# Performance work log

Measured on AMD Instinct MI355X. Metric: run time of the kernel, lower is better.

## Reference

```python
import jax, jax.numpy as jnp
import numpy as np
import math

ROPE_THETA = 10000.0

def apply_rope(t, pos, theta):
    # t: [b, h, s, d_k] with d_k even; pos: [b, s] int
    d_k = t.shape[-1]
    inv_freq = theta ** (-jnp.arange(0, d_k, 2, dtype=jnp.float32) / d_k)  # [d_k/2]
    angles = pos.astype(jnp.float32)[..., None] * inv_freq  # [b, s, d_k/2]
    cos = jnp.cos(angles)[:, None, :, :]  # [b, 1, s, d_k/2]
    sin = jnp.sin(angles)[:, None, :, :]
    t_even = t[..., 0::2]
    t_odd = t[..., 1::2]
    out_even = cos * t_even - sin * t_odd
    out_odd = sin * t_even + cos * t_odd
    # interleave back: [..., d_k/2, 2] -> [..., d_k]
    return jnp.stack([out_even, out_odd], axis=-1).reshape(t.shape)

def setup_inputs() -> dict:
    key = jax.random.key(0)
    k1, k2, k3, k4, k5 = jax.random.split(key, 5)
    b, s, d_model = 2, 2048, 1024
    std = math.sqrt(2.0 / (2 * d_model))
    return {
        "x": jax.random.normal(k1, (b, s, d_model), dtype=jnp.float32),
        "token_positions": jnp.broadcast_to(jnp.arange(s, dtype=jnp.int32), (b, s)),
        "W_Q": jax.random.normal(k2, (d_model, d_model), dtype=jnp.float32) * std,
        "W_K": jax.random.normal(k3, (d_model, d_model), dtype=jnp.float32) * std,
        "W_V": jax.random.normal(k4, (d_model, d_model), dtype=jnp.float32) * std,
        "W_O": jax.random.normal(k5, (d_model, d_model), dtype=jnp.float32) * std,
    }

def reference(x, token_positions, W_Q, W_K, W_V, W_O):
    b, s, d_model = x.shape
    n_heads = 16
    d_k = d_model // n_heads

    def proj(W):
        # x @ W^T then split heads: [b, s, d_model] -> [b, h, s, d_k]
        y = jnp.einsum('bsd,ed->bse', x, W)
        return y.reshape(b, s, n_heads, d_k).transpose(0, 2, 1, 3)

    Q = apply_rope(proj(W_Q), token_positions, ROPE_THETA)
    K = apply_rope(proj(W_K), token_positions, ROPE_THETA)
    V = proj(W_V)

    scores = jnp.einsum('bhqd,bhkd->bhqk', Q, K) / math.sqrt(d_k)
    causal = jnp.tril(jnp.ones((s, s), dtype=bool))  # True = keep
    scores = jnp.where(causal, scores, -jnp.inf)
    attn = jax.nn.softmax(scores, axis=-1)
    out = jnp.einsum('bhqk,bhkd->bhqd', attn, V)
    out = out.transpose(0, 2, 1, 3).reshape(b, s, d_model)  # merge heads
    return jnp.einsum('bse,de->bsd', out, W_O)
```

## Files before the change

### kernel.cpp

```cpp
#include <hip/hip_runtime.h>
#include <hip/hip_bf16.h>

typedef __attribute__((ext_vector_type(8))) short short8;
typedef __attribute__((ext_vector_type(4))) short short4v;
typedef __attribute__((ext_vector_type(4))) float f32x4;

#define LN10000_DIV32 0.2878231366242558f
#define SCALE_Q_LOG2E 0.18033688011112042f
#define EXP_BIAS 12.0f

__device__ __forceinline__ unsigned short f2bf(float f){
  union { float fv; unsigned u; } a; a.fv = f;
  return (unsigned short)((a.u + 0x7fffu + ((a.u >> 16) & 1u)) >> 16);
}

__global__ __launch_bounds__(256) void convert_all(
    const float* __restrict__ x, const float* __restrict__ wq,
    const float* __restrict__ wk, const float* __restrict__ wv,
    const float* __restrict__ wo, unsigned short* __restrict__ dst,
    float2* __restrict__ tab)
{
  size_t t = (size_t)blockIdx.x * 256 + threadIdx.x;
  if (t < 65536UL){
    const int s = (int)(t >> 5), ip = (int)(t & 31);
    float invf = __expf(-(float)ip * LN10000_DIV32);
    float ang = (float)s * invf;
    tab[t] = make_float2(__cosf(ang), __sinf(ang));
  }
  size_t e = t * 8;
  const float* src; size_t off;
  if (e < 4194304UL)      { src = x;  off = e; }
  else if (e < 5242880UL) { src = wq; off = e - 4194304UL; }
  else if (e < 6291456UL) { src = wk; off = e - 5242880UL; }
  else if (e < 7340032UL) { src = wv; off = e - 6291456UL; }
  else                    { src = wo; off = e - 7340032UL; }
  float4 f0 = *(const float4*)(src + off);
  float4 f1 = *(const float4*)(src + off + 4);
  short8 o;
  o[0] = (short)f2bf(f0.x); o[1] = (short)f2bf(f0.y);
  o[2] = (short)f2bf(f0.z); o[3] = (short)f2bf(f0.w);
  o[4] = (short)f2bf(f1.x); o[5] = (short)f2bf(f1.y);
  o[6] = (short)f2bf(f1.z); o[7] = (short)f2bf(f1.w);
  *(short8*)(dst + e) = o;
}

__global__ __launch_bounds__(512, 2) void gemm_qkv(
    const unsigned short* __restrict__ Xb, const unsigned short* __restrict__ Wb,
    const int* __restrict__ positions, const float2* __restrict__ tab,
    unsigned short* __restrict__ Qb, unsigned short* __restrict__ Kb,
    unsigned short* __restrict__ Vtb)
{
  __shared__ __align__(16) unsigned short As[2*8192];
  __shared__ __align__(16) unsigned short Bs[2*12288];
  f32x4 acc[4][3] = {};
  const int tid = threadIdx.x, lane = tid & 63, w = tid >> 6;
  const int wm = w >> 2, wn = w & 3;
  const int fr = lane & 15, fq = lane >> 4;
  const int id  = blockIdx.x;
  const int xcd = id & 7;
  const int lid = id >> 3;
  const int m0 = (lid & 31) * 128;
  const int n0 = (xcd*2 + (lid >> 5)) * 192;

#define STAGE_ALL(kt, buf) do {                                                     \
    _Pragma("unroll")                                                               \
    for (int i_ = 0; i_ < 2; ++i_){                             \
      const int c_ = i_*512 + tid;                                                  \
      const int row_ = c_ >> 3, cd_ = c_ & 7;                                       \
      const int sc_ = (cd_ ^ (row_ & 7)) << 3;                                      \
      const unsigned short* ga_ = Xb + (size_t)(m0 + row_) * 1024 + (kt)*64 + sc_;  \
      __builtin_amdgcn_global_load_lds((const __attribute__((address_space(1))) void*)ga_, \
          (__attribute__((address_space(3))) void*)(As + (buf)*8192 + c_*8), 16, 0, 0);    \
    }                                                                               \
    _Pragma("unroll")                                                               \
    for (int i_ = 0; i_ < 3; ++i_){                             \
      const int c_ = i_*512 + tid;                                                  \
      const int row_ = c_ >> 3, cd_ = c_ & 7;                                       \
      const int sc_ = (cd_ ^ (row_ & 7)) << 3;                                      \
      const unsigned short* gb_ = Wb + (size_t)(n0 + row_) * 1024 + (kt)*64 + sc_;  \
      __builtin_amdgcn_global_load_lds((const __attribute__((address_space(1))) void*)gb_, \
          (__attribute__((address_space(3))) void*)(Bs + (buf)*12288 + c_*8), 16, 0, 0);   \
    }                                                                               \
  } while(0)

  STAGE_ALL(0, 0);

  const int row_a0 = wm*64 + fr;
  const int row_b0 = wn*48 + fr;

  for (int t = 0; t < 16; ++t){
    const int cur = t & 1;
    if (t + 1 < 16){
      STAGE_ALL(t + 1, cur ^ 1);
      asm volatile("s_waitcnt vmcnt(5)" ::: "memory");
    } else {
      asm volatile("s_waitcnt vmcnt(0)" ::: "memory");
    }
    __builtin_amdgcn_s_barrier();
    asm volatile("" ::: "memory");
    const unsigned short* as = As + cur*8192;
    const unsigned short* bs = Bs + cur*12288;
    short8 af[4], bfv[3];

#define LDA(mf_, kh_) do { \
      const int row_ = row_a0 + (mf_)*16; \
      const int c_ = ((kh_)*4 + fq) ^ (row_ & 7); \
      af[mf_] = *(const short8*)(as + row_*64 + c_*8); } while(0)
#define LDB(nf_, kh_) do { \
      const int row_ = row_b0 + (nf_)*16; \
      const int c_ = ((kh_)*4 + fq) ^ (row_ & 7); \
      bfv[nf_] = *(const short8*)(bs + row_*64 + c_*8); } while(0)

    LDA(0,0); LDA(1,0); LDA(2,0); LDA(3,0);
    LDB(0,0); LDB(1,0); LDB(2,0);
    __builtin_amdgcn_s_setprio(1);
    #pragma unroll
    for (int mf = 0; mf < 4; ++mf)
      #pragma unroll
      for (int nf = 0; nf < 3; ++nf)
        acc[mf][nf] = __builtin_amdgcn_mfma_f32_16x16x32_bf16(af[mf], bfv[nf], acc[mf][nf], 0, 0, 0);
    __builtin_amdgcn_s_setprio(0);

    LDA(0,1); LDA(1,1); LDA(2,1); LDA(3,1);
    LDB(0,1); LDB(1,1); LDB(2,1);
    __builtin_amdgcn_s_setprio(1);
    #pragma unroll
    for (int mf = 0; mf < 4; ++mf)
      #pragma unroll
      for (int nf = 0; nf < 3; ++nf)
        acc[mf][nf] = __builtin_amdgcn_mfma_f32_16x16x32_bf16(af[mf], bfv[nf], acc[mf][nf], 0, 0, 0);
    __builtin_amdgcn_s_setprio(0);
    asm volatile("" ::: "memory");
    __builtin_amdgcn_s_barrier();
#undef LDA
#undef LDB
  }
#undef STAGE_ALL

  #pragma unroll
  for (int mf = 0; mf < 4; ++mf){
    int pm[4];
    #pragma unroll
    for (int r = 0; r < 4; ++r){
      const int m = m0 + wm*64 + mf*16 + fq*4 + r;
      pm[r] = positions[m] & 2047;
    }
    const int mbase = m0 + wm*64 + mf*16 + fq*4;
    const int b = mbase >> 11;
    const int s0 = mbase & 2047;
    #pragma unroll
    for (int nf = 0; nf < 3; ++nf){
      const int n = n0 + wn*48 + nf*16 + fr;
      const int seg = n >> 10;
      const int h = (n & 1023) >> 6, d = n & 63;
      const size_t bh = (size_t)b * 16 + h;
      if (seg == 2){
        short4v pack;
        #pragma unroll
        for (int r = 0; r < 4; ++r)
          pack[r] = (short)f2bf(acc[mf][nf][r]);
        *(short4v*)&Vtb[(bh*64 + d)*2048 + s0] = pack;
      } else {
        const int ip = d >> 1;
        #pragma unroll
        for (int r = 0; r < 4; ++r){
          float v = acc[mf][nf][r];
          float pv = __shfl_xor(v, 1);
          const float2 cs = tab[(pm[r] << 5) + ip];
          float outv = (d & 1) ? (cs.x * v + cs.y * pv)
                               : (cs.x * v - cs.y * pv);
          if (seg == 0) outv *= SCALE_Q_LOG2E;
          const unsigned short ob = f2bf(outv);
          const int s = s0 + r;
          if (seg == 0) Qb[(bh*2048 + s)*64 + d] = ob;
          else          Kb[(bh*2048 + s)*64 + d] = ob;
        }
      }
    }
  }
}

__global__ __launch_bounds__(256) void attn_kernel(
    const unsigned short* __restrict__ Qb, const unsigned short* __restrict__ Kb,
    const unsigned short* __restrict__ Vtb, unsigned short* __restrict__ Ob)
{
  __shared__ __align__(16) unsigned short Ks[2][4096];
  __shared__ __align__(16) unsigned short Vs[2][4096];
  __shared__ __align__(16) unsigned short Plds[4][16][64];

  const int tid = threadIdx.x, lane = tid & 63, w = tid >> 6;
  const int fr = lane & 15, fq = lane >> 4;

  const int i = blockIdx.x;
  const int bh = (i & 7) | (((i >> 3) & 3) << 3);
  const int tile = 31 - (i >> 5);
  const int b = bh >> 4, h = bh & 15;
  const int q0 = tile * 64 + w * 16;
  const size_t qk_base = (size_t)bh * 2048 * 64;
  const unsigned short* kbase = Kb + qk_base;
  const unsigned short* vbase = Vtb + (size_t)bh * 64 * 2048;

  const unsigned short* qp = Qb + qk_base + (size_t)(q0 + fr) * 64 + fq * 8;
  short8 aq0 = *(const short8*)qp;
  short8 aq1 = *(const short8*)(qp + 32);

  f32x4 accO[4] = {};
  float lrun = 0.f;
  const int qrow = q0 + fr;
  const int nt = tile + 1;
  const int sw3 = (fr & 7) << 2;

#define STAGE_KV(t_, buf_) do {                                                     \
    const int kv0_ = (t_) * 64;                                                     \
    _Pragma("unroll")                                                               \
    for (int ii_ = 0; ii_ < 2; ++ii_){                                              \
      const int chunk_ = ii_ * 256 + tid;                                           \
      const int row_ = chunk_ >> 3, cd_ = chunk_ & 7;                               \
      const int sc_ = (cd_ ^ (row_ & 7)) << 3;                                      \
      const unsigned short* ksrc_ = kbase + (size_t)(kv0_ + row_) * 64 + sc_;       \
      const unsigned short* vsrc_ = vbase + (size_t)row_ * 2048 + kv0_ + sc_;       \
      __builtin_amdgcn_global_load_lds((const __attribute__((address_space(1))) void*)ksrc_, \
          (__attribute__((address_space(3))) void*)(&Ks[buf_][0] + chunk_*8), 16, 0, 0);     \
      __builtin_amdgcn_global_load_lds((const __attribute__((address_space(1))) void*)vsrc_, \
          (__attribute__((address_space(3))) void*)(&Vs[buf_][0] + chunk_*8), 16, 0, 0);     \
    }                                                                               \
  } while(0)

  STAGE_KV(0, 0);
  for (int t = 0; t < nt; ++t){
    const int cur = t & 1;
    const int kv0 = t * 64;
    if (t + 1 < nt){
      STAGE_KV(t + 1, cur ^ 1);
      asm volatile("s_waitcnt vmcnt(4)" ::: "memory");
    } else {
      asm volatile("s_waitcnt vmcnt(0)" ::: "memory");
    }
    __builtin_amdgcn_s_barrier();
    asm volatile("" ::: "memory");
    const unsigned short* ks = &Ks[cur][0];
    const unsigned short* vs = &Vs[cur][0];

    f32x4 sT[4];
    #pragma unroll
    for (int kf = 0; kf < 4; ++kf){
      const int row = kf*16 + fr;
      const int swr = row & 7;
      short8 k0 = *(const short8*)(ks + row*64 + ((fq ^ swr) << 3));
      short8 k1 = *(const short8*)(ks + row*64 + (((4 + fq) ^ swr) << 3));
      f32x4 s = {0.f, 0.f, 0.f, 0.f};
      s = __builtin_amdgcn_mfma_f32_16x16x32_bf16(k0, aq0, s, 0, 0, 0);
      s = __builtin_amdgcn_mfma_f32_16x16x32_bf16(k1, aq1, s, 0, 0, 0);
      sT[kf] = s;
    }
    if (t == nt - 1){
      #pragma unroll
      for (int kf = 0; kf < 4; ++kf)
        #pragma unroll
        for (int r = 0; r < 4; ++r){
          const int kvcol = kv0 + kf*16 + fq*4 + r;
          if (kvcol > qrow) sT[kf][r] = -1e30f;
        }
    }
    float p[4][4];
    float rs = 0.f;
    #pragma unroll
    for (int kf = 0; kf < 4; ++kf)
      #pragma unroll
      for (int r = 0; r < 4; ++r){
        p[kf][r] = __builtin_amdgcn_exp2f(sT[kf][r] - EXP_BIAS);
        rs += p[kf][r];
      }
    rs += __shfl_xor(rs, 16);
    rs += __shfl_xor(rs, 32);
    lrun += rs;
    unsigned* prow = (unsigned*)&Plds[w][fr][0];
    #pragma unroll
    for (int kf = 0; kf < 4; ++kf)
      #pragma unroll
      for (int jj = 0; jj < 2; ++jj){
        unsigned pk;
        asm("v_cvt_pk_bf16_f32 %0, %1, %2" : "=v"(pk) : "v"(p[kf][2*jj]), "v"(p[kf][2*jj+1]));
        prow[(kf*8 + fq*2 + jj) ^ sw3] = pk;
      }
    asm volatile("s_waitcnt lgkmcnt(0)" ::: "memory");
    const unsigned* crow = (const unsigned*)&Plds[w][fr][0];
    short8 ap0 = *(const short8*)&crow[(fq*4) ^ sw3];
    short8 ap1 = *(const short8*)&crow[(16 + fq*4) ^ sw3];
    __builtin_amdgcn_s_setprio(1);
    #pragma unroll
    for (int dblk = 0; dblk < 4; ++dblk){
      const int d = dblk*16 + fr;
      const int swd = d & 7;
      short8 bv0 = *(const short8*)(vs + d*64 + ((fq ^ swd) << 3));
      short8 bv1 = *(const short8*)(vs + d*64 + (((4 + fq) ^ swd) << 3));
      accO[dblk] = __builtin_amdgcn_mfma_f32_16x16x32_bf16(ap0, bv0, accO[dblk], 0, 0, 0);
      accO[dblk] = __builtin_amdgcn_mfma_f32_16x16x32_bf16(ap1, bv1, accO[dblk], 0, 0, 0);
    }
    __builtin_amdgcn_s_setprio(0);
    asm volatile("" ::: "memory");
    __builtin_amdgcn_s_barrier();
  }
#undef STAGE_KV
  float lq[4];
  #pragma unroll
  for (int r = 0; r < 4; ++r)
    lq[r] = __shfl(lrun, fq*4 + r);
  #pragma unroll
  for (int dblk = 0; dblk < 4; ++dblk)
    #pragma unroll
    for (int r = 0; r < 4; ++r){
      const int s = q0 + fq*4 + r;
      const float o = accO[dblk][r] / lq[r];
      Ob[((size_t)b*2048 + s)*1024 + h*64 + dblk*16 + fr] = f2bf(o);
    }
}

__global__ __launch_bounds__(256, 2) void gemm_out(
    const unsigned short* __restrict__ Obf, const unsigned short* __restrict__ Wb,
    float* __restrict__ out)
{
  __shared__ __align__(16) unsigned short As[2*8192];
  __shared__ __align__(16) unsigned short Bs[2*4096];
  f32x4 acc[4][2] = {};
  const int tid = threadIdx.x, lane = tid & 63, w = tid >> 6;
  const int wm = w >> 1, wn = w & 1;
  const int fr = lane & 15, fq = lane >> 4;
  const int id  = blockIdx.x;
  const int xcd = id & 7;
  const int lid = id >> 3;
  const int m0 = (xcd*4 + (lid & 3)) * 128;
  const int n0 = (lid >> 2) * 64;

#define STAGEO(kt, buf) do {                                                        \
    _Pragma("unroll")                                                               \
    for (int i_ = 0; i_ < 4; ++i_){                             \
      const int c_ = i_*256 + tid;                                                  \
      const int row_ = c_ >> 3, cd_ = c_ & 7;                                       \
      const int sc_ = (cd_ ^ (row_ & 7)) << 3;                                      \
      const unsigned short* ga_ = Obf + (size_t)(m0 + row_) * 1024 + (kt)*64 + sc_; \
      __builtin_amdgcn_global_load_lds((const __attribute__((address_space(1))) void*)ga_, \
          (__attribute__((address_space(3))) void*)(As + (buf)*8192 + c_*8), 16, 0, 0);    \
    }                                                                               \
    _Pragma("unroll")                                                               \
    for (int i_ = 0; i_ < 2; ++i_){                              \
      const int c_ = i_*256 + tid;                                                  \
      const int row_ = c_ >> 3, cd_ = c_ & 7;                                       \
      const int sc_ = (cd_ ^ (row_ & 7)) << 3;                                      \
      const unsigned short* gb_ = Wb + (size_t)(n0 + row_) * 1024 + (kt)*64 + sc_;  \
      __builtin_amdgcn_global_load_lds((const __attribute__((address_space(1))) void*)gb_, \
          (__attribute__((address_space(3))) void*)(Bs + (buf)*4096 + c_*8), 16, 0, 0);    \
    }                                                                               \
  } while(0)

  STAGEO(0, 0);

  const int row_a0 = wm*64 + fr;
  const int row_b0 = wn*32 + fr;

  for (int t = 0; t < 16; ++t){
    const int cur = t & 1;
    if (t + 1 < 16){
      STAGEO(t + 1, cur ^ 1);
      asm volatile("s_waitcnt vmcnt(6)" ::: "memory");
    } else {
      asm volatile("s_waitcnt vmcnt(0)" ::: "memory");
    }
    __builtin_amdgcn_s_barrier();
    asm volatile("" ::: "memory");
    const unsigned short* as = As + cur*8192;
    const unsigned short* bs = Bs + cur*4096;
    short8 af[4], bfv[2];

#define LDA(mf_, kh_) do { \
      const int row_ = row_a0 + (mf_)*16; \
      const int c_ = ((kh_)*4 + fq) ^ (row_ & 7); \
      af[mf_] = *(const short8*)(as + row_*64 + c_*8); } while(0)
#define LDB(nf_, kh_) do { \
      const int row_ = row_b0 + (nf_)*16; \
      const int c_ = ((kh_)*4 + fq) ^ (row_ & 7); \
      bfv[nf_] = *(const short8*)(bs + row_*64 + c_*8); } while(0)

    LDA(0,0); LDA(1,0); LDA(2,0); LDA(3,0);
    LDB(0,0); LDB(1,0);
    __builtin_amdgcn_s_setprio(1);
    #pragma unroll
    for (int mf = 0; mf < 4; ++mf)
      #pragma unroll
      for (int nf = 0; nf < 2; ++nf)
        acc[mf][nf] = __builtin_amdgcn_mfma_f32_16x16x32_bf16(af[mf], bfv[nf], acc[mf][nf], 0, 0, 0);
    __builtin_amdgcn_s_setprio(0);

    LDA(0,1); LDA(1,1); LDA(2,1); LDA(3,1);
    LDB(0,1); LDB(1,1);
    __builtin_amdgcn_s_setprio(1);
    #pragma unroll
    for (int mf = 0; mf < 4; ++mf)
      #pragma unroll
      for (int nf = 0; nf < 2; ++nf)
        acc[mf][nf] = __builtin_amdgcn_mfma_f32_16x16x32_bf16(af[mf], bfv[nf], acc[mf][nf], 0, 0, 0);
    __builtin_amdgcn_s_setprio(0);
    asm volatile("" ::: "memory");
    __builtin_amdgcn_s_barrier();
#undef LDA
#undef LDB
  }
#undef STAGEO

  #pragma unroll
  for (int mf = 0; mf < 4; ++mf)
    #pragma unroll
    for (int nf = 0; nf < 2; ++nf){
      const int n = n0 + wn*32 + nf*16 + fr;
      #pragma unroll
      for (int r = 0; r < 4; ++r){
        const int m = m0 + wm*64 + mf*16 + fq*4 + r;
        out[(size_t)m * 1024 + n] = acc[mf][nf][r];
      }
    }
}

extern "C" void kernel_launch(void* const* d_in, const int* in_sizes, int n_in,
                              void* d_out, int out_size, void* d_ws, size_t ws_size,
                              hipStream_t stream) {
  const float* x  = (const float*)d_in[0];
  const int* pos  = (const int*)d_in[1];
  const float* wq = (const float*)d_in[2];
  const float* wk = (const float*)d_in[3];
  const float* wv = (const float*)d_in[4];
  const float* wo = (const float*)d_in[5];
  float* out = (float*)d_out;

  unsigned short* ws = (unsigned short*)d_ws;
  unsigned short* Xb   = ws;
  unsigned short* Wqkv = ws + 4194304UL;
  unsigned short* Wo   = ws + 7340032UL;
  unsigned short* Qb   = ws + 8388608UL;
  unsigned short* Kb   = ws + 12582912UL;
  unsigned short* Vt   = ws + 16777216UL;
  unsigned short* Ob   = ws + 20971520UL;
  float2* tab          = (float2*)(ws + 25165824UL);

  convert_all<<<4096, 256, 0, stream>>>(x, wq, wk, wv, wo, ws, tab);

  gemm_qkv<<<512, 512, 0, stream>>>(Xb, Wqkv, pos, tab, Qb, Kb, Vt);

  attn_kernel<<<1024, 256, 0, stream>>>(Qb, Kb, Vt, Ob);

  gemm_out<<<512, 256, 0, stream>>>(Ob, Wo, out);
}
```

Measured before the change: 100.1 us.

## Split long causal attention rows across two KV chunks and combine partials

```diff
diff --git a/kernel.cpp b/kernel.cpp
--- a/kernel.cpp
+++ b/kernel.cpp
@@ -64,7 +64,7 @@
 
 #define STAGE_ALL(kt, buf) do {                                                     \
     _Pragma("unroll")                                                               \
-    for (int i_ = 0; i_ < 2; ++i_){                             \
+    for (int i_ = 0; i_ < 2; ++i_){                                                 \
       const int c_ = i_*512 + tid;                                                  \
       const int row_ = c_ >> 3, cd_ = c_ & 7;                                       \
       const int sc_ = (cd_ ^ (row_ & 7)) << 3;                                      \
@@ -73,7 +73,7 @@
           (__attribute__((address_space(3))) void*)(As + (buf)*8192 + c_*8), 16, 0, 0);    \
     }                                                                               \
     _Pragma("unroll")                                                               \
-    for (int i_ = 0; i_ < 3; ++i_){                             \
+    for (int i_ = 0; i_ < 3; ++i_){                                                 \
       const int c_ = i_*512 + tid;                                                  \
       const int row_ = c_ >> 3, cd_ = c_ & 7;                                       \
       const int sc_ = (cd_ ^ (row_ & 7)) << 3;                                      \
@@ -182,7 +182,8 @@
 
 __global__ __launch_bounds__(256) void attn_kernel(
     const unsigned short* __restrict__ Qb, const unsigned short* __restrict__ Kb,
-    const unsigned short* __restrict__ Vtb, unsigned short* __restrict__ Ob)
+    const unsigned short* __restrict__ Vtb, unsigned short* __restrict__ Ob,
+    float* __restrict__ Opart, float* __restrict__ lpart)
 {
   __shared__ __align__(16) unsigned short Ks[2][4096];
   __shared__ __align__(16) unsigned short Vs[2][4096];
@@ -193,9 +194,24 @@
 
   const int i = blockIdx.x;
   const int bh = (i & 7) | (((i >> 3) & 3) << 3);
-  const int tile = 31 - (i >> 5);
+  const int slot = i >> 5;
+  int qtile, kv_begin, kv_end, chunk, two_chunk;
+  if (slot < 32){
+    qtile = 31 - (slot >> 1);
+    chunk = slot & 1;
+    const int ntq = qtile + 1;
+    const int c0 = ntq - (ntq >> 1);
+    kv_begin = chunk ? c0 : 0;
+    kv_end   = chunk ? ntq : c0;
+    two_chunk = 1;
+  } else {
+    qtile = 47 - slot;
+    chunk = 0;
+    kv_begin = 0; kv_end = qtile + 1;
+    two_chunk = 0;
+  }
   const int b = bh >> 4, h = bh & 15;
-  const int q0 = tile * 64 + w * 16;
+  const int q0 = qtile * 64 + w * 16;
   const size_t qk_base = (size_t)bh * 2048 * 64;
   const unsigned short* kbase = Kb + qk_base;
   const unsigned short* vbase = Vtb + (size_t)bh * 64 * 2048;
@@ -207,7 +223,6 @@
   f32x4 accO[4] = {};
   float lrun = 0.f;
   const int qrow = q0 + fr;
-  const int nt = tile + 1;
   const int sw3 = (fr & 7) << 2;
 
 #define STAGE_KV(t_, buf_) do {                                                     \
@@ -226,11 +241,11 @@
     }                                                                               \
   } while(0)
 
-  STAGE_KV(0, 0);
-  for (int t = 0; t < nt; ++t){
-    const int cur = t & 1;
+  STAGE_KV(kv_begin, 0);
+  for (int t = kv_begin; t < kv_end; ++t){
+    const int cur = (t - kv_begin) & 1;
     const int kv0 = t * 64;
-    if (t + 1 < nt){
+    if (t + 1 < kv_end){
       STAGE_KV(t + 1, cur ^ 1);
       asm volatile("s_waitcnt vmcnt(4)" ::: "memory");
     } else {
@@ -253,7 +268,7 @@
       s = __builtin_amdgcn_mfma_f32_16x16x32_bf16(k1, aq1, s, 0, 0, 0);
       sT[kf] = s;
     }
-    if (t == nt - 1){
+    if (t == qtile){
       #pragma unroll
       for (int kf = 0; kf < 4; ++kf)
         #pragma unroll
@@ -302,18 +317,66 @@
     __builtin_amdgcn_s_barrier();
   }
 #undef STAGE_KV
-  float lq[4];
+
+  if (!two_chunk){
+    float lq[4];
+    #pragma unroll
+    for (int r = 0; r < 4; ++r)
+      lq[r] = __shfl(lrun, fq*4 + r);
+    #pragma unroll
+    for (int dblk = 0; dblk < 4; ++dblk)
+      #pragma unroll
+      for (int r = 0; r < 4; ++r){
+        const int s = q0 + fq*4 + r;
+        const float o = accO[dblk][r] / lq[r];
+        Ob[((size_t)b*2048 + s)*1024 + h*64 + dblk*16 + fr] = f2bf(o);
+      }
+  } else {
+    #pragma unroll
+    for (int dblk = 0; dblk < 4; ++dblk)
+      #pragma unroll
+      for (int r = 0; r < 4; ++r){
+        const int s = q0 + fq*4 + r;
+        Opart[(((size_t)chunk*32 + bh)*1024 + (s - 1024))*64 + dblk*16 + fr] = accO[dblk][r];
+      }
+    if (fq == 0)
+      lpart[((size_t)chunk*32 + bh)*1024 + (qrow - 1024)] = lrun;
+  }
+}
+
+__global__ __launch_bounds__(256) void attn_combine(
+    const float* __restrict__ Opart, const float* __restrict__ lpart,
+    unsigned short* __restrict__ Ob)
+{
+  const int gid = blockIdx.x * 256 + threadIdx.x;
+  const int row = gid >> 2;
+  const int d0  = (gid & 3) * 16;
+  const int bh = row >> 10;
+  const int srow = 1024 + (row & 1023);
+  const int b = bh >> 4, h = bh & 15;
+  const float l = lpart[row] + lpart[32*1024 + row];
+  const float inv = 1.f / l;
+  const float* p0 = Opart + ((size_t)row)*64 + d0;
+  const float* p1 = Opart + ((size_t)(32*1024) + row)*64 + d0;
+  short8 o01[2];
   #pragma unroll
-  for (int r = 0; r < 4; ++r)
-    lq[r] = __shfl(lrun, fq*4 + r);
-  #pragma unroll
-  for (int dblk = 0; dblk < 4; ++dblk)
-    #pragma unroll
-    for (int r = 0; r < 4; ++r){
-      const int s = q0 + fq*4 + r;
-      const float o = accO[dblk][r] / lq[r];
-      Ob[((size_t)b*2048 + s)*1024 + h*64 + dblk*16 + fr] = f2bf(o);
-    }
+  for (int g = 0; g < 2; ++g){
+    float4 a0 = *(const float4*)(p0 + g*8);
+    float4 a1 = *(const float4*)(p1 + g*8);
+    float4 b0 = *(const float4*)(p0 + g*8 + 4);
+    float4 b1 = *(const float4*)(p1 + g*8 + 4);
+    o01[g][0] = (short)f2bf((a0.x + a1.x) * inv);
+    o01[g][1] = (short)f2bf((a0.y + a1.y) * inv);
+    o01[g][2] = (short)f2bf((a0.z + a1.z) * inv);
+    o01[g][3] = (short)f2bf((a0.w + a1.w) * inv);
+    o01[g][4] = (short)f2bf((b0.x + b1.x) * inv);
+    o01[g][5] = (short)f2bf((b0.y + b1.y) * inv);
+    o01[g][6] = (short)f2bf((b0.z + b1.z) * inv);
+    o01[g][7] = (short)f2bf((b0.w + b1.w) * inv);
+  }
+  unsigned short* dst = Ob + ((size_t)b*2048 + srow)*1024 + h*64 + d0;
+  *(short8*)(dst)     = o01[0];
+  *(short8*)(dst + 8) = o01[1];
 }
 
 __global__ __launch_bounds__(256, 2) void gemm_out(
@@ -334,7 +397,7 @@
 
 #define STAGEO(kt, buf) do {                                                        \
     _Pragma("unroll")                                                               \
-    for (int i_ = 0; i_ < 4; ++i_){                             \
+    for (int i_ = 0; i_ < 4; ++i_){                                                 \
       const int c_ = i_*256 + tid;                                                  \
       const int row_ = c_ >> 3, cd_ = c_ & 7;                                       \
       const int sc_ = (cd_ ^ (row_ & 7)) << 3;                                      \
@@ -343,7 +406,7 @@
           (__attribute__((address_space(3))) void*)(As + (buf)*8192 + c_*8), 16, 0, 0);    \
     }                                                                               \
     _Pragma("unroll")                                                               \
-    for (int i_ = 0; i_ < 2; ++i_){                              \
+    for (int i_ = 0; i_ < 2; ++i_){                                                 \
       const int c_ = i_*256 + tid;                                                  \
       const int row_ = c_ >> 3, cd_ = c_ & 7;                                       \
       const int sc_ = (cd_ ^ (row_ & 7)) << 3;                                      \
@@ -440,12 +503,16 @@
   unsigned short* Vt   = ws + 16777216UL;
   unsigned short* Ob   = ws + 20971520UL;
   float2* tab          = (float2*)(ws + 25165824UL);
+  float* Opart         = (float*)(ws + 25427968UL);
+  float* lpart         = Opart + 4194304UL;
 
   convert_all<<<4096, 256, 0, stream>>>(x, wq, wk, wv, wo, ws, tab);
 
   gemm_qkv<<<512, 512, 0, stream>>>(Xb, Wqkv, pos, tab, Qb, Kb, Vt);
 
-  attn_kernel<<<1024, 256, 0, stream>>>(Qb, Kb, Vt, Ob);
+  attn_kernel<<<1536, 256, 0, stream>>>(Qb, Kb, Vt, Ob, Opart, lpart);
+
+  attn_combine<<<512, 256, 0, stream>>>(Opart, lpart, Ob);
 
   gemm_out<<<512, 256, 0, stream>>>(Ob, Wo, out);
 }
```

New measurement: 115.3 us. 15.1% more time.
